# Performance work log

Hardware: AMD Instinct MI355X
Metric: run time of the kernel (lower is better)

Reference implementation:

```python
import jax, jax.numpy as jnp
import numpy as np

N, E, G = 50000, 800000, 64
L, C, IN, H, OUT = 3, 4, 64, 64, 64
BN_EPS = 1e-5


def setup_inputs() -> dict:
    key = jax.random.key(0)
    ks = jax.random.split(key, 12)
    x = jax.random.normal(ks[0], (N, IN), dtype=jnp.float32)
    cluster_labels = jax.random.randint(ks[1], (N,), 0, C, dtype=jnp.int32)
    edge_index = jax.random.randint(ks[2], (2, E), 0, N, dtype=jnp.int64)
    batch = jnp.sort(jax.random.randint(ks[3], (N,), 0, G, dtype=jnp.int64))
    s1 = 1.0 / np.sqrt(H)
    # per (layer, cluster) GIN MLP params: Lin(H,H) -> BN -> ReLU -> Lin(H,H)
    W1 = jax.random.normal(ks[4], (L, C, H, H), dtype=jnp.float32) * s1
    b1 = jnp.zeros((L, C, H), dtype=jnp.float32)
    g1 = jnp.ones((L, C, H), dtype=jnp.float32)
    be1 = jnp.zeros((L, C, H), dtype=jnp.float32)
    W2 = jax.random.normal(ks[5], (L, C, H, H), dtype=jnp.float32) * s1
    b2 = jnp.zeros((L, C, H), dtype=jnp.float32)
    # pool MLP: Lin(H*L, H) -> BN -> ReLU -> Lin(H, OUT)
    Wp1 = jax.random.normal(ks[6], (H * L, H), dtype=jnp.float32) / np.sqrt(H * L)
    bp1 = jnp.zeros((H,), dtype=jnp.float32)
    gp = jnp.ones((H,), dtype=jnp.float32)
    bep = jnp.zeros((H,), dtype=jnp.float32)
    Wp2 = jax.random.normal(ks[7], (H, OUT), dtype=jnp.float32) * s1
    bp2 = jnp.zeros((OUT,), dtype=jnp.float32)
    return {"x": x, "cluster_labels": cluster_labels, "edge_index": edge_index,
            "batch": batch, "W1": W1, "b1": b1, "g1": g1, "be1": be1,
            "W2": W2, "b2": b2, "Wp1": Wp1, "bp1": bp1, "gp": gp,
            "bep": bep, "Wp2": Wp2, "bp2": bp2}


def _masked_bn(h, mf, gamma, beta):
    # BatchNorm computed only over rows where mask is set (those are the rows fed to nn)
    cnt = jnp.maximum(mf.sum(), 1.0)
    mean = (mf[:, None] * h).sum(0) / cnt
    var = (mf[:, None] * (h - mean) ** 2).sum(0) / cnt
    return (h - mean) * jax.lax.rsqrt(var + BN_EPS) * gamma + beta


def _bn(h, gamma, beta):
    mean = h.mean(0)
    var = ((h - mean) ** 2).mean(0)
    return (h - mean) * jax.lax.rsqrt(var + BN_EPS) * gamma + beta


def reference(x, cluster_labels, edge_index, batch, W1, b1, g1, be1, W2, b2,
              Wp1, bp1, gp, bep, Wp2, bp2):
    src, dst = edge_index[0], edge_index[1]
    pooled = []
    for t in range(L):
        for c in range(C):
            mask = cluster_labels == c
            mf = mask.astype(x.dtype)
            # GIN aggregation: out[i] = sum_{j -> i} x[j]
            agg = jax.ops.segment_sum(x[src], dst, num_segments=N)
            h = agg + x  # (1 + eps) * x residual with eps = 0
            h = h @ W1[t, c] + b1[t, c]
            h = jax.nn.relu(_masked_bn(h, mf, g1[t, c], be1[t, c]))
            h = h @ W2[t, c] + b2[t, c]
            x = jnp.where(mask[:, None], h, x)
        pooled.append(jax.ops.segment_sum(x, batch, num_segments=G))
    z = jnp.concatenate(pooled, axis=1)  # [G, H*L]
    z = z @ Wp1 + bp1
    z = jax.nn.relu(_bn(z, gp, bep))
    return z @ Wp2 + bp2
```

## Files before the change

kernel.cpp:

```cpp
#include <hip/hip_runtime.h>
#include <hip/hip_bf16.h>

#define NN 50000
#define EE 800000
#define GG 64
#define LL 3
#define CC 4
#define HH 64
#define BN_EPS 1e-5f
#define NSHADOW 4
#define SBLK 196
#define GIN_BLOCKS 2048


__device__ __forceinline__ float bcast(float v, int j) {
    return __int_as_float(__builtin_amdgcn_readlane(__float_as_int(v), j));
}


__global__ void k_deghist(const int* __restrict__ dst, int* __restrict__ deg,
                          const int* __restrict__ labels, int* __restrict__ blockcnt,
                          const float* __restrict__ x_in, __hip_bfloat16* __restrict__ xw) {
    __shared__ int cnt[CC];
    int tid = threadIdx.x;
    for (int i = blockIdx.x * 256 + tid; i < NN * 64; i += gridDim.x * 256)
        xw[i] = __float2bfloat16(x_in[i]);
    bool hist = (blockIdx.x < SBLK);
    if (hist && tid < CC) cnt[tid] = 0;
    __syncthreads();
    int gid = blockIdx.x * 256 + tid;
    if (gid < EE) atomicAdd(&deg[dst[gid]], 1);
    if (hist && gid < NN) atomicAdd(&cnt[labels[gid]], 1);
    __syncthreads();
    if (hist && tid < CC) blockcnt[tid * SBLK + blockIdx.x] = cnt[tid];
}

__global__ __launch_bounds__(256) void k_scancombo(
    const int* __restrict__ deg, int* __restrict__ rowptr, int* __restrict__ dpart,
    const int* __restrict__ blockcnt, int* __restrict__ coffs, int* __restrict__ ccount) {
    __shared__ int smem[CC * 256];
    int tid = threadIdx.x;
    if (blockIdx.x < SBLK) {
        int i = blockIdx.x * 256 + tid;
        int v = (i < NN) ? deg[i] : 0;
        smem[tid] = v;
        __syncthreads();
        for (int off = 1; off < 256; off <<= 1) {
            int u = (tid >= off) ? smem[tid - off] : 0;
            __syncthreads();
            smem[tid] += u;
            __syncthreads();
        }
        if (i < NN) rowptr[i] = smem[tid] - v;
        if (tid == 255) dpart[blockIdx.x] = smem[255];
    } else {
        int own[CC];
        for (int c = 0; c < CC; c++) {
            own[c] = (tid < SBLK) ? blockcnt[c * SBLK + tid] : 0;
            smem[c * 256 + tid] = own[c];
        }
        __syncthreads();
        for (int off = 1; off < 256; off <<= 1) {
            int v[CC];
            for (int c = 0; c < CC; c++) v[c] = (tid >= off) ? smem[c * 256 + tid - off] : 0;
            __syncthreads();
            for (int c = 0; c < CC; c++) smem[c * 256 + tid] += v[c];
            __syncthreads();
        }
        if (tid < SBLK)
            for (int c = 0; c < CC; c++) coffs[c * SBLK + tid] = smem[c * 256 + tid] - own[c];
        if (tid == 0)
            for (int c = 0; c < CC; c++) ccount[c] = smem[c * 256 + 255];
    }
}

__global__ __launch_bounds__(256) void k_dscan2(int* __restrict__ dpart,
                                                int* __restrict__ dbase,
                                                int* __restrict__ rowptr) {
    __shared__ int s[256];
    int tid = threadIdx.x;
    int v = (tid < SBLK) ? dpart[tid] : 0;
    s[tid] = v;
    __syncthreads();
    for (int off = 1; off < 256; off <<= 1) {
        int u = (tid >= off) ? s[tid - off] : 0;
        __syncthreads();
        s[tid] += u;
        __syncthreads();
    }
    if (tid < SBLK) dbase[tid] = s[tid] - v;
    if (tid == 0) rowptr[NN] = EE;
}

__global__ __launch_bounds__(256) void k_cfill_dscan3(
    int* __restrict__ rowptr, const int* __restrict__ dbase, int* __restrict__ cursor,
    const int* __restrict__ labels, const int* __restrict__ coffs, int* __restrict__ clist) {
    __shared__ int pos[CC];
    int tid = threadIdx.x;
    if (tid < CC) pos[tid] = coffs[tid * SBLK + blockIdx.x];
    __syncthreads();
    int i = blockIdx.x * 256 + tid;
    if (i < NN) {
        int r = rowptr[i] + dbase[blockIdx.x];
        rowptr[i] = r;
        cursor[i] = r;
        int c = labels[i];
        int p = atomicAdd(&pos[c], 1);
        clist[c * NN + p] = i;
    }
}

__global__ void k_fill(const int* __restrict__ src, const int* __restrict__ dst,
                       int* __restrict__ cursor, int* __restrict__ adj) {
    int e = blockIdx.x * blockDim.x + threadIdx.x;
    if (e < EE) {
        int d = dst[e];
        int pos = atomicAdd(&cursor[d], 1);
        adj[pos] = src[e] << 7;
    }
}

__global__ __launch_bounds__(256) void k_gin_a(
    const __hip_bfloat16* __restrict__ xw, const int* __restrict__ adj,
    const int* __restrict__ rowptr, const int* __restrict__ clist_c,
    const int* __restrict__ ccount_c, const float* __restrict__ W1,
    const float* __restrict__ b1, __hip_bfloat16* __restrict__ h1buf,
    float* __restrict__ bnacc,
    const int* __restrict__ batch, float* __restrict__ z, int tpool) {
    __shared__ float lds_red[4][128];
    int cnt = *ccount_c;
    int lane = threadIdx.x & 63;
    int wave = threadIdx.x >> 6;
    int nwaves = gridDim.x * 4;
    const char* xwb = (const char*)xw;
    float sS = 0.f, sQ = 0.f;
    int idx = blockIdx.x * 4 + wave;
    int node_next = (idx < cnt) ? clist_c[idx] : 0;
    for (; idx < cnt; idx += nwaves) {
        int node = node_next;
        int nidx = idx + nwaves;
        if (nidx < cnt) node_next = clist_c[nidx];
        int rb = rowptr[node], re = rowptr[node + 1];
        float a0 = __bfloat162float(xw[(size_t)node * 64 + lane]);
        float a1 = 0.f, a2 = 0.f, a3 = 0.f, a4 = 0.f, a5 = 0.f, a6 = 0.f, a7 = 0.f;
        int base = rb, rem = re - rb;
        while (rem > 0) {
            int take = min(rem, 64);
            int nb = adj[base + min(lane, take - 1)];
            int j = 0;
            for (; j + 8 <= take; j += 8) {
                int o0 = __builtin_amdgcn_readlane(nb, j + 0);
                int o1 = __builtin_amdgcn_readlane(nb, j + 1);
                int o2 = __builtin_amdgcn_readlane(nb, j + 2);
                int o3 = __builtin_amdgcn_readlane(nb, j + 3);
                int o4 = __builtin_amdgcn_readlane(nb, j + 4);
                int o5 = __builtin_amdgcn_readlane(nb, j + 5);
                int o6 = __builtin_amdgcn_readlane(nb, j + 6);
                int o7 = __builtin_amdgcn_readlane(nb, j + 7);
                a0 += __bfloat162float(((const __hip_bfloat16*)(xwb + o0))[lane]);
                a1 += __bfloat162float(((const __hip_bfloat16*)(xwb + o1))[lane]);
                a2 += __bfloat162float(((const __hip_bfloat16*)(xwb + o2))[lane]);
                a3 += __bfloat162float(((const __hip_bfloat16*)(xwb + o3))[lane]);
                a4 += __bfloat162float(((const __hip_bfloat16*)(xwb + o4))[lane]);
                a5 += __bfloat162float(((const __hip_bfloat16*)(xwb + o5))[lane]);
                a6 += __bfloat162float(((const __hip_bfloat16*)(xwb + o6))[lane]);
                a7 += __bfloat162float(((const __hip_bfloat16*)(xwb + o7))[lane]);
            }
            for (; j < take; j++) {
                int o = __builtin_amdgcn_readlane(nb, j);
                a0 += __bfloat162float(((const __hip_bfloat16*)(xwb + o))[lane]);
            }
            base += take; rem -= take;
        }
        float acc = ((a0 + a1) + (a2 + a3)) + ((a4 + a5) + (a6 + a7));
        float s = b1[lane];
        #pragma unroll
        for (int j = 0; j < 64; j++) s += bcast(acc, j) * W1[j * 64 + lane];
        __hip_bfloat16 hb = __float2bfloat16(s);
        h1buf[(size_t)idx * 64 + lane] = hb;
        float st = __bfloat162float(hb);
        sS += st; sQ += st * st;
    }
    lds_red[wave][lane] = sS;
    lds_red[wave][64 + lane] = sQ;
    __syncthreads();
    if (threadIdx.x < 128) {
        float v = lds_red[0][threadIdx.x] + lds_red[1][threadIdx.x] +
                  lds_red[2][threadIdx.x] + lds_red[3][threadIdx.x];
        atomicAdd(&bnacc[(blockIdx.x & (NSHADOW - 1)) * 128 + threadIdx.x], v);
    }
    if (tpool >= 0) {
        int wid = blockIdx.x * 4 + wave;
        int lo = wid * 64;
        if (lo < NN) {
            int hi = min(lo + 64, NN);
            float acc = 0.f;
            int curg = batch[lo];
            for (int n = lo; n < hi; n++) {
                int g = batch[n];
                if (g != curg) {
                    atomicAdd(&z[curg * (HH * LL) + tpool * HH + lane], acc);
                    acc = 0.f;
                    curg = g;
                }
                acc += __bfloat162float(xw[(size_t)n * 64 + lane]);
            }
            atomicAdd(&z[curg * (HH * LL) + tpool * HH + lane], acc);
        }
    }
}

__global__ __launch_bounds__(256) void k_gin_c(
    __hip_bfloat16* __restrict__ xw, const int* __restrict__ clist_c,
    const int* __restrict__ ccount_c, const float* __restrict__ g1,
    const float* __restrict__ be1, const float* __restrict__ W2,
    const float* __restrict__ b2, const __hip_bfloat16* __restrict__ h1buf,
    const float* __restrict__ bnacc) {
    __shared__ float lds_scale[64];
    __shared__ float lds_shift[64];
    int cnt = *ccount_c;
    int lane = threadIdx.x & 63;
    int wave = threadIdx.x >> 6;
    if (threadIdx.x < 64) {
        float s = 0.f, q = 0.f;
        #pragma unroll
        for (int sh = 0; sh < NSHADOW; sh++) {
            s += bnacc[sh * 128 + threadIdx.x];
            q += bnacc[sh * 128 + 64 + threadIdx.x];
        }
        float fc = fmaxf((float)cnt, 1.f);
        float mean = s / fc;
        float var = q / fc - mean * mean;
        float sc = g1[threadIdx.x] * rsqrtf(var + BN_EPS);
        lds_scale[threadIdx.x] = sc;
        lds_shift[threadIdx.x] = be1[threadIdx.x] - mean * sc;
    }
    __syncthreads();
    int nwaves = gridDim.x * 4;
    for (int idx = blockIdx.x * 4 + wave; idx < cnt; idx += nwaves) {
        float h = __bfloat162float(h1buf[(size_t)idx * 64 + lane]);
        float a = fmaxf(h * lds_scale[lane] + lds_shift[lane], 0.f);
        float s = b2[lane];
        #pragma unroll
        for (int j = 0; j < 64; j++) s += bcast(a, j) * W2[j * 64 + lane];
        xw[(size_t)clist_c[idx] * 64 + lane] = __float2bfloat16(s);
    }
}

__global__ void k_pool(const __hip_bfloat16* __restrict__ xw, const int* __restrict__ batch,
                       float* __restrict__ z, int t) {
    const int CHUNK = 64;
    int lane = threadIdx.x & 63;
    int wg = (blockIdx.x * blockDim.x + threadIdx.x) >> 6;
    int lo = wg * CHUNK;
    if (lo >= NN) return;
    int hi = min(lo + CHUNK, NN);
    float acc = 0.f;
    int curg = batch[lo];
    for (int n = lo; n < hi; n++) {
        int g = batch[n];
        if (g != curg) {
            atomicAdd(&z[curg * (HH * LL) + t * HH + lane], acc);
            acc = 0.f;
            curg = g;
        }
        acc += __bfloat162float(xw[(size_t)n * 64 + lane]);
    }
    atomicAdd(&z[curg * (HH * LL) + t * HH + lane], acc);
}

__global__ __launch_bounds__(256) void k_final1(
    const float* __restrict__ z, const float* __restrict__ Wp1,
    const float* __restrict__ bp1, float* __restrict__ hbuf) {
    __shared__ float red[256];
    int g = blockIdx.x;
    int k = threadIdx.x & 63;
    int part = threadIdx.x >> 6;
    float s = 0.f;
    #pragma unroll 8
    for (int j = part * 48; j < (part + 1) * 48; j++)
        s += z[g * (HH * LL) + j] * Wp1[j * 64 + k];
    red[threadIdx.x] = s;
    __syncthreads();
    if (part == 0)
        hbuf[g * 64 + k] = red[k] + red[64 + k] + red[128 + k] + red[192 + k] + bp1[k];
}

__global__ __launch_bounds__(256) void k_final2(
    const float* __restrict__ hbuf, const float* __restrict__ gp,
    const float* __restrict__ bep, const float* __restrict__ Wp2,
    const float* __restrict__ bp2, float* __restrict__ out) {
    __shared__ float lds[64 * 64];
    __shared__ float sscale[64];
    __shared__ float sshift[64];
    int tid = threadIdx.x;
    for (int i = tid; i < 64 * 64; i += 256) lds[i] = hbuf[i];
    __syncthreads();
    if (tid < 64) {
        float s = 0.f, q = 0.f;
        for (int g = 0; g < 64; g++) { float v = lds[g * 64 + tid]; s += v; q += v * v; }
        float mean = s / 64.f;
        float var = q / 64.f - mean * mean;
        float sc = gp[tid] * rsqrtf(var + BN_EPS);
        sscale[tid] = sc;
        sshift[tid] = bep[tid] - mean * sc;
    }
    __syncthreads();
    for (int i = tid; i < 64 * 64; i += 256) {
        int k = i & 63;
        lds[i] = fmaxf(lds[i] * sscale[k] + sshift[k], 0.f);
    }
    __syncthreads();
    for (int i = tid; i < 64 * 64; i += 256) {
        int g = i >> 6, o = i & 63;
        float s = bp2[o];
        #pragma unroll 8
        for (int k = 0; k < 64; k++) s += lds[g * 64 + k] * Wp2[k * 64 + o];
        out[g * 64 + o] = s;
    }
}

extern "C" void kernel_launch(void* const* d_in, const int* in_sizes, int n_in,
                              void* d_out, int out_size, void* d_ws, size_t ws_size,
                              hipStream_t stream) {
    const float* x_in = (const float*)d_in[0];
    const int* labels = (const int*)d_in[1];
    const int* esrc = (const int*)d_in[2];
    const int* edst = esrc + EE;
    const int* batch = (const int*)d_in[3];
    const float* W1 = (const float*)d_in[4];
    const float* b1 = (const float*)d_in[5];
    const float* g1 = (const float*)d_in[6];
    const float* be1 = (const float*)d_in[7];
    const float* W2 = (const float*)d_in[8];
    const float* b2 = (const float*)d_in[9];
    const float* Wp1 = (const float*)d_in[10];
    const float* bp1 = (const float*)d_in[11];
    const float* gp = (const float*)d_in[12];
    const float* bep = (const float*)d_in[13];
    const float* Wp2 = (const float*)d_in[14];
    const float* bp2 = (const float*)d_in[15];
    float* out = (float*)d_out;

    char* p = (char*)d_ws;
    auto carve = [&](size_t bytes) -> void* {
        void* r = (void*)p;
        p += (bytes + 255) & ~(size_t)255;
        return r;
    };
    float* bnacc = (float*)carve((size_t)LL * CC * NSHADOW * 128 * 4);
    float* z     = (float*)carve((size_t)GG * HH * LL * 4);
    int*   deg   = (int*)carve((size_t)NN * 4);
    size_t zero_bytes = (size_t)(p - (char*)d_ws);
    int*   ccount  = (int*)carve(CC * 4);
    int*   blockcnt= (int*)carve((size_t)CC * SBLK * 4);
    int*   coffs   = (int*)carve((size_t)CC * SBLK * 4);
    int*   dpart   = (int*)carve((size_t)SBLK * 4);
    int*   dbase   = (int*)carve((size_t)SBLK * 4);
    __hip_bfloat16* xw    = (__hip_bfloat16*)carve((size_t)NN * 64 * 2);
    __hip_bfloat16* h1buf = (__hip_bfloat16*)carve((size_t)NN * 64 * 2);
    float* hbuf    = (float*)carve((size_t)GG * 64 * 4);
    int*   rowptr  = (int*)carve((size_t)(NN + 1) * 4);
    int*   cursor  = (int*)carve((size_t)NN * 4);
    int*   adj     = (int*)carve((size_t)EE * 4);
    int*   clist   = (int*)carve((size_t)CC * NN * 4);

    hipMemsetAsync(d_ws, 0, zero_bytes, stream);

    k_deghist<<<(EE + 255) / 256, 256, 0, stream>>>(edst, deg, labels, blockcnt, x_in, xw);
    k_scancombo<<<SBLK + 1, 256, 0, stream>>>(deg, rowptr, dpart, blockcnt, coffs, ccount);
    k_dscan2<<<1, 256, 0, stream>>>(dpart, dbase, rowptr);
    k_cfill_dscan3<<<SBLK, 256, 0, stream>>>(rowptr, dbase, cursor, labels, coffs, clist);
    k_fill<<<(EE + 255) / 256, 256, 0, stream>>>(esrc, edst, cursor, adj);

    for (int t = 0; t < LL; t++) {
        for (int c = 0; c < CC; c++) {
            int tc = t * CC + c;
            int tpool = (c == 0) ? (t - 1) : -1;
            k_gin_a<<<GIN_BLOCKS, 256, 0, stream>>>(
                xw, adj, rowptr, clist + c * NN, ccount + c,
                W1 + (size_t)tc * 4096, b1 + (size_t)tc * 64, h1buf,
                bnacc + (size_t)tc * NSHADOW * 128, batch, z, tpool);
            k_gin_c<<<GIN_BLOCKS, 256, 0, stream>>>(
                xw, clist + c * NN, ccount + c,
                g1 + (size_t)tc * 64, be1 + (size_t)tc * 64,
                W2 + (size_t)tc * 4096, b2 + (size_t)tc * 64, h1buf,
                bnacc + (size_t)tc * NSHADOW * 128);
        }
    }
    {
        int pool_waves = (NN + 63) / 64;
        int pool_blocks = (pool_waves * 64 + 255) / 256;
        k_pool<<<pool_blocks, 256, 0, stream>>>(xw, batch, z, LL - 1);
    }
    k_final1<<<GG, 256, 0, stream>>>(z, Wp1, bp1, hbuf);
    k_final2<<<1, 256, 0, stream>>>(hbuf, gp, bep, Wp2, bp2, out);
}
```

Measured before the change: 646.3 us.

## Split GIN gather from linears and run both MLP matmuls on bf16 MFMA

Splits the fused gather-plus-Lin1 kernel into a pure neighbour-gather kernel that writes bf16 aggregates, and a separate Lin1 kernel. Lin1 and Lin2 now run as 16x16x32 bf16 MFMA tiles on 16-row tiles instead of per-node readlane broadcast FMAs. A new prepack kernel converts W1 and W2 into MFMA fragment layout in bf16. The aim is to replace scalar broadcast matmul work with matrix-core instructions. In exchange it adds an extra kernel launch per cluster step, an extra round trip of the aggregate buffer through memory, and bf16 rounding of the aggregate before Lin1.

```diff
diff --git a/kernel.cpp b/kernel.cpp
--- a/kernel.cpp
+++ b/kernel.cpp
@@ -11,10 +11,18 @@
 #define NSHADOW 4
 #define SBLK 196
 #define GIN_BLOCKS 2048
-
-
-__device__ __forceinline__ float bcast(float v, int j) {
-    return __int_as_float(__builtin_amdgcn_readlane(__float_as_int(v), j));
+#define MM_BLOCKS 256
+
+
+typedef __attribute__((ext_vector_type(8))) short bf16x8;
+typedef __attribute__((ext_vector_type(4))) float f32x4;
+
+__device__ __forceinline__ float bf2f(short s) {
+    return __int_as_float(((int)(unsigned short)s) << 16);
+}
+__device__ __forceinline__ short f2bf(float v) {
+    __hip_bfloat16 hb = __float2bfloat16(v);
+    return *(short*)&hb;
 }
 
 
@@ -33,6 +41,22 @@
     if (hist && gid < NN) atomicAdd(&cnt[labels[gid]], 1);
     __syncthreads();
     if (hist && tid < CC) blockcnt[tid * SBLK + blockIdx.x] = cnt[tid];
+}
+
+__global__ void k_wpack(const float* __restrict__ W1, const float* __restrict__ W2,
+                        short* __restrict__ wf) {
+    int o = blockIdx.x * 256 + threadIdx.x;
+    if (o >= 24 * 4096) return;
+    int m = o >> 12;
+    int r = o & 4095;
+    int colt = r >> 10;
+    int fragk = (r >> 9) & 1;
+    int lane = (r >> 3) & 63;
+    int j = r & 7;
+    int k = fragk * 32 + ((lane >> 4) << 3) + j;
+    int n = colt * 16 + (lane & 15);
+    const float* src = (m < 12) ? (W1 + (size_t)m * 4096) : (W2 + (size_t)(m - 12) * 4096);
+    wf[o] = f2bf(src[k * 64 + n]);
 }
 
 __global__ __launch_bounds__(256) void k_scancombo(
@@ -120,21 +144,18 @@
     }
 }
 
-__global__ __launch_bounds__(256) void k_gin_a(
+__global__ __launch_bounds__(256) void k_gather(
     const __hip_bfloat16* __restrict__ xw, const int* __restrict__ adj,
     const int* __restrict__ rowptr, const int* __restrict__ clist_c,
-    const int* __restrict__ ccount_c, const float* __restrict__ W1,
-    const float* __restrict__ b1, __hip_bfloat16* __restrict__ h1buf,
-    float* __restrict__ bnacc,
+    const int* __restrict__ ccount_c, __hip_bfloat16* __restrict__ aggbuf,
     const int* __restrict__ batch, float* __restrict__ z, int tpool) {
-    __shared__ float lds_red[4][128];
     int cnt = *ccount_c;
     int lane = threadIdx.x & 63;
     int wave = threadIdx.x >> 6;
+    int wid = blockIdx.x * 4 + wave;
     int nwaves = gridDim.x * 4;
     const char* xwb = (const char*)xw;
-    float sS = 0.f, sQ = 0.f;
-    int idx = blockIdx.x * 4 + wave;
+    int idx = wid;
     int node_next = (idx < cnt) ? clist_c[idx] : 0;
     for (; idx < cnt; idx += nwaves) {
         int node = node_next;
@@ -173,24 +194,9 @@
             base += take; rem -= take;
         }
         float acc = ((a0 + a1) + (a2 + a3)) + ((a4 + a5) + (a6 + a7));
-        float s = b1[lane];
-        #pragma unroll
-        for (int j = 0; j < 64; j++) s += bcast(acc, j) * W1[j * 64 + lane];
-        __hip_bfloat16 hb = __float2bfloat16(s);
-        h1buf[(size_t)idx * 64 + lane] = hb;
-        float st = __bfloat162float(hb);
-        sS += st; sQ += st * st;
-    }
-    lds_red[wave][lane] = sS;
-    lds_red[wave][64 + lane] = sQ;
-    __syncthreads();
-    if (threadIdx.x < 128) {
-        float v = lds_red[0][threadIdx.x] + lds_red[1][threadIdx.x] +
-                  lds_red[2][threadIdx.x] + lds_red[3][threadIdx.x];
-        atomicAdd(&bnacc[(blockIdx.x & (NSHADOW - 1)) * 128 + threadIdx.x], v);
+        aggbuf[(size_t)idx * 64 + lane] = __float2bfloat16(acc);
     }
     if (tpool >= 0) {
-        int wid = blockIdx.x * 4 + wave;
         int lo = wid * 64;
         if (lo < NN) {
             int hi = min(lo + 64, NN);
@@ -210,17 +216,87 @@
     }
 }
 
-__global__ __launch_bounds__(256) void k_gin_c(
+__global__ __launch_bounds__(256) void k_lin1(
+    const __hip_bfloat16* __restrict__ aggbuf, const int* __restrict__ ccount_c,
+    const short* __restrict__ wf1, const float* __restrict__ b1c,
+    __hip_bfloat16* __restrict__ h1buf, float* __restrict__ bnacc) {
+    int cnt = *ccount_c;
+    int tiles = (cnt + 15) >> 4;
+    int lane = threadIdx.x & 63;
+    int wave = threadIdx.x >> 6;
+    int wid = blockIdx.x * 4 + wave;
+    int nwaves = gridDim.x * 4;
+    int quad = lane >> 4;
+    int l15 = lane & 15;
+
+    bf16x8 wb[8];
+    #pragma unroll
+    for (int f = 0; f < 8; f++)
+        wb[f] = *(const bf16x8*)(wf1 + f * 512 + lane * 8);
+    float bcol[4];
+    #pragma unroll
+    for (int colt = 0; colt < 4; colt++) bcol[colt] = b1c[colt * 16 + l15];
+
+    float sS[4] = {0.f, 0.f, 0.f, 0.f};
+    float sQ[4] = {0.f, 0.f, 0.f, 0.f};
+
+    for (int tile = wid; tile < tiles; tile += nwaves) {
+        int tb = tile << 4;
+        int row = tb + l15;
+        const __hip_bfloat16* ar = aggbuf + (size_t)row * 64 + quad * 8;
+        bf16x8 a0 = *(const bf16x8*)ar;
+        bf16x8 a1 = *(const bf16x8*)(ar + 32);
+        #pragma unroll
+        for (int colt = 0; colt < 4; colt++) {
+            f32x4 acc = {0.f, 0.f, 0.f, 0.f};
+            acc = __builtin_amdgcn_mfma_f32_16x16x32_bf16(a0, wb[colt * 2 + 0], acc, 0, 0, 0);
+            acc = __builtin_amdgcn_mfma_f32_16x16x32_bf16(a1, wb[colt * 2 + 1], acc, 0, 0, 0);
+            #pragma unroll
+            for (int r = 0; r < 4; r++) {
+                int nrow = tb + quad * 4 + r;
+                if (nrow < cnt) {
+                    float s = acc[r] + bcol[colt];
+                    __hip_bfloat16 hb = __float2bfloat16(s);
+                    h1buf[(size_t)nrow * 64 + colt * 16 + l15] = hb;
+                    float st = __bfloat162float(hb);
+                    sS[colt] += st;
+                    sQ[colt] += st * st;
+                }
+            }
+        }
+    }
+    #pragma unroll
+    for (int colt = 0; colt < 4; colt++) {
+        sS[colt] += __shfl_xor(sS[colt], 16); sS[colt] += __shfl_xor(sS[colt], 32);
+        sQ[colt] += __shfl_xor(sQ[colt], 16); sQ[colt] += __shfl_xor(sQ[colt], 32);
+    }
+    if (quad == 0) {
+        int slot = (blockIdx.x & (NSHADOW - 1)) * 128;
+        #pragma unroll
+        for (int colt = 0; colt < 4; colt++) {
+            atomicAdd(&bnacc[slot + colt * 16 + l15], sS[colt]);
+            atomicAdd(&bnacc[slot + 64 + colt * 16 + l15], sQ[colt]);
+        }
+    }
+}
+
+__global__ __launch_bounds__(256) void k_cmfma(
     __hip_bfloat16* __restrict__ xw, const int* __restrict__ clist_c,
-    const int* __restrict__ ccount_c, const float* __restrict__ g1,
-    const float* __restrict__ be1, const float* __restrict__ W2,
-    const float* __restrict__ b2, const __hip_bfloat16* __restrict__ h1buf,
+    const int* __restrict__ ccount_c, const float* __restrict__ g1c,
+    const float* __restrict__ be1c, const short* __restrict__ wf2,
+    const float* __restrict__ b2c, const __hip_bfloat16* __restrict__ h1buf,
     const float* __restrict__ bnacc) {
     __shared__ float lds_scale[64];
     __shared__ float lds_shift[64];
     int cnt = *ccount_c;
+    int tiles = (cnt + 15) >> 4;
     int lane = threadIdx.x & 63;
     int wave = threadIdx.x >> 6;
+    int wid = blockIdx.x * 4 + wave;
+    int nwaves = gridDim.x * 4;
+    int quad = lane >> 4;
+    int l15 = lane & 15;
+
     if (threadIdx.x < 64) {
         float s = 0.f, q = 0.f;
         #pragma unroll
@@ -231,19 +307,54 @@
         float fc = fmaxf((float)cnt, 1.f);
         float mean = s / fc;
         float var = q / fc - mean * mean;
-        float sc = g1[threadIdx.x] * rsqrtf(var + BN_EPS);
+        float sc = g1c[threadIdx.x] * rsqrtf(var + BN_EPS);
         lds_scale[threadIdx.x] = sc;
-        lds_shift[threadIdx.x] = be1[threadIdx.x] - mean * sc;
-    }
-    __syncthreads();
-    int nwaves = gridDim.x * 4;
-    for (int idx = blockIdx.x * 4 + wave; idx < cnt; idx += nwaves) {
-        float h = __bfloat162float(h1buf[(size_t)idx * 64 + lane]);
-        float a = fmaxf(h * lds_scale[lane] + lds_shift[lane], 0.f);
-        float s = b2[lane];
+        lds_shift[threadIdx.x] = be1c[threadIdx.x] - mean * sc;
+    }
+    __syncthreads();
+
+    bf16x8 wb[8];
+    #pragma unroll
+    for (int f = 0; f < 8; f++)
+        wb[f] = *(const bf16x8*)(wf2 + f * 512 + lane * 8);
+    float bcol[4];
+    #pragma unroll
+    for (int colt = 0; colt < 4; colt++) bcol[colt] = b2c[colt * 16 + l15];
+    float scl0[8], sft0[8], scl1[8], sft1[8];
+    #pragma unroll
+    for (int j = 0; j < 8; j++) {
+        int ch = quad * 8 + j;
+        scl0[j] = lds_scale[ch];      sft0[j] = lds_shift[ch];
+        scl1[j] = lds_scale[ch + 32]; sft1[j] = lds_shift[ch + 32];
+    }
+
+    for (int tile = wid; tile < tiles; tile += nwaves) {
+        int tb = tile << 4;
+        int row = tb + l15;
+        const __hip_bfloat16* hr = h1buf + (size_t)row * 64 + quad * 8;
+        bf16x8 h0 = *(const bf16x8*)hr;
+        bf16x8 h1f = *(const bf16x8*)(hr + 32);
+        bf16x8 a0, a1;
         #pragma unroll
-        for (int j = 0; j < 64; j++) s += bcast(a, j) * W2[j * 64 + lane];
-        xw[(size_t)clist_c[idx] * 64 + lane] = __float2bfloat16(s);
+        for (int j = 0; j < 8; j++) {
+            a0[j] = f2bf(fmaxf(bf2f(h0[j]) * scl0[j] + sft0[j], 0.f));
+            a1[j] = f2bf(fmaxf(bf2f(h1f[j]) * scl1[j] + sft1[j], 0.f));
+        }
+        #pragma unroll
+        for (int colt = 0; colt < 4; colt++) {
+            f32x4 acc = {0.f, 0.f, 0.f, 0.f};
+            acc = __builtin_amdgcn_mfma_f32_16x16x32_bf16(a0, wb[colt * 2 + 0], acc, 0, 0, 0);
+            acc = __builtin_amdgcn_mfma_f32_16x16x32_bf16(a1, wb[colt * 2 + 1], acc, 0, 0, 0);
+            #pragma unroll
+            for (int r = 0; r < 4; r++) {
+                int nrow = tb + quad * 4 + r;
+                if (nrow < cnt) {
+                    int node = clist_c[nrow];
+                    xw[(size_t)node * 64 + colt * 16 + l15] =
+                        __float2bfloat16(acc[r] + bcol[colt]);
+                }
+            }
+        }
     }
 }
 
@@ -357,8 +468,10 @@
     int*   coffs   = (int*)carve((size_t)CC * SBLK * 4);
     int*   dpart   = (int*)carve((size_t)SBLK * 4);
     int*   dbase   = (int*)carve((size_t)SBLK * 4);
-    __hip_bfloat16* xw    = (__hip_bfloat16*)carve((size_t)NN * 64 * 2);
-    __hip_bfloat16* h1buf = (__hip_bfloat16*)carve((size_t)NN * 64 * 2);
+    __hip_bfloat16* xw     = (__hip_bfloat16*)carve((size_t)NN * 64 * 2);
+    __hip_bfloat16* aggbuf = (__hip_bfloat16*)carve((size_t)NN * 64 * 2);
+    __hip_bfloat16* h1buf  = (__hip_bfloat16*)carve((size_t)NN * 64 * 2);
+    short* wf      = (short*)carve((size_t)24 * 4096 * 2);
     float* hbuf    = (float*)carve((size_t)GG * 64 * 4);
     int*   rowptr  = (int*)carve((size_t)(NN + 1) * 4);
     int*   cursor  = (int*)carve((size_t)NN * 4);
@@ -368,6 +481,7 @@
     hipMemsetAsync(d_ws, 0, zero_bytes, stream);
 
     k_deghist<<<(EE + 255) / 256, 256, 0, stream>>>(edst, deg, labels, blockcnt, x_in, xw);
+    k_wpack<<<(24 * 4096 + 255) / 256, 256, 0, stream>>>(W1, W2, wf);
     k_scancombo<<<SBLK + 1, 256, 0, stream>>>(deg, rowptr, dpart, blockcnt, coffs, ccount);
     k_dscan2<<<1, 256, 0, stream>>>(dpart, dbase, rowptr);
     k_cfill_dscan3<<<SBLK, 256, 0, stream>>>(rowptr, dbase, cursor, labels, coffs, clist);
@@ -377,15 +491,16 @@
         for (int c = 0; c < CC; c++) {
             int tc = t * CC + c;
             int tpool = (c == 0) ? (t - 1) : -1;
-            k_gin_a<<<GIN_BLOCKS, 256, 0, stream>>>(
-                xw, adj, rowptr, clist + c * NN, ccount + c,
-                W1 + (size_t)tc * 4096, b1 + (size_t)tc * 64, h1buf,
-                bnacc + (size_t)tc * NSHADOW * 128, batch, z, tpool);
-            k_gin_c<<<GIN_BLOCKS, 256, 0, stream>>>(
+            k_gather<<<GIN_BLOCKS, 256, 0, stream>>>(
+                xw, adj, rowptr, clist + c * NN, ccount + c, aggbuf, batch, z, tpool);
+            k_lin1<<<MM_BLOCKS, 256, 0, stream>>>(
+                aggbuf, ccount + c, wf + (size_t)tc * 4096, b1 + (size_t)tc * 64,
+                h1buf, bnacc + (size_t)tc * NSHADOW * 128);
+            k_cmfma<<<MM_BLOCKS, 256, 0, stream>>>(
                 xw, clist + c * NN, ccount + c,
                 g1 + (size_t)tc * 64, be1 + (size_t)tc * 64,
-                W2 + (size_t)tc * 4096, b2 + (size_t)tc * 64, h1buf,
-                bnacc + (size_t)tc * NSHADOW * 128);
+                wf + (size_t)(12 + tc) * 4096, b2 + (size_t)tc * 64,
+                h1buf, bnacc + (size_t)tc * NSHADOW * 128);
         }
     }
     {
```

Result: faster. 563.4 us (-12.8%).
